# Performance work log

Measured on AMD Instinct MI355X. Metric: run time of the kernel, lower is better.

The kernel has to match this reference:

```python
import jax, jax.numpy as jnp
import numpy as np

B, S, E, H, D, W = 2, 4096, 768, 12, 64, 256  # batch, seq, hidden, heads, head_dim, one-sided window


def setup_inputs() -> dict:
    key = jax.random.key(0)
    ks = jax.random.split(key, 4)
    s = 0.02
    return {
        "hidden_states": jax.random.normal(ks[0], (B, S, E), jnp.float32),
        "Wq": jax.random.normal(ks[1], (E, E), jnp.float32) * s,
        "bq": jnp.zeros((E,), jnp.float32),
        "Wk": jax.random.normal(ks[2], (E, E), jnp.float32) * s,
        "bk": jnp.zeros((E,), jnp.float32),
        "Wv": jax.random.normal(ks[3], (E, E), jnp.float32) * s,
        "bv": jnp.zeros((E,), jnp.float32),
    }


def _band_attention(q, k, v):
    # q,k,v: [B,H,S,D]. Sliding-window attention: query i attends keys j with |j-i| <= W,
    # clipped to [0, S) -- same math as sliding_chunks_matmul_qk + mask_invalid_locations
    # + softmax + sliding_chunks_matmul_pv (dropout p=0, eval mode).
    C = S // W  # number of query chunks of size W

    def ext(x):
        # gather, for each chunk c, the keys of chunks c-1, c, c+1 (zero padded at edges)
        xp = jnp.pad(x, ((0, 0), (0, 0), (W, W), (0, 0)))
        xc = xp.reshape(B, H, C + 2, W, D)
        return jnp.concatenate([xc[:, :, 0:C], xc[:, :, 1:C + 1], xc[:, :, 2:C + 2]], axis=3)  # [B,H,C,3W,D]

    qc = q.reshape(B, H, C, W, D)
    ke = ext(k)
    ve = ext(v)
    scores = jnp.einsum('bhcpd,bhctd->bhcpt', qc, ke)  # [B,H,C,W,3W]

    p = jnp.arange(W)[:, None]            # query offset within chunk
    t = jnp.arange(3 * W)[None, :]        # key offset within extended window
    rel = t - W - p                       # j - i  (relative position)
    j = jnp.arange(C)[:, None, None] * W + (t - W)[None]  # global key index [C,W,3W]
    mask = (jnp.abs(rel)[None] <= W) & (j >= 0) & (j < S)  # band + sequence-boundary mask

    scores = jnp.where(mask[None, None], scores, -1e30)
    probs = jax.nn.softmax(scores, axis=-1)
    out = jnp.einsum('bhcpt,bhctd->bhcpd', probs, ve)
    return out.reshape(B, H, S, D)


def reference(hidden_states, Wq, bq, Wk, bk, Wv, bv):
    scale = 1.0 / float(np.sqrt(D))
    q = (hidden_states @ Wq + bq) * scale  # q scaled by 1/sqrt(head_dim) as in original
    k = hidden_states @ Wk + bk
    v = hidden_states @ Wv + bv
    split = lambda x: x.reshape(B, S, H, D).transpose(0, 2, 1, 3)  # [B,H,S,D]
    out = _band_attention(split(q), split(k), split(v))
    return out.transpose(0, 2, 1, 3).reshape(B, S, E)  # [B,S,E] context_layer
```

## Files before the change

kernel.cpp:

```cpp
#include <hip/hip_runtime.h>

#define BB 2
#define SS 4096
#define EE 768
#define HH 12
#define DD 64
#define WW 256

typedef __attribute__((ext_vector_type(8))) short short8;
typedef __attribute__((ext_vector_type(4))) short short4v;
typedef __attribute__((ext_vector_type(4))) float floatx4;

#define MFMA16(a, b, c) __builtin_amdgcn_mfma_f32_16x16x32_bf16(a, b, c, 0, 0, 0)

__device__ __forceinline__ float bf2f(short x) {
    union { unsigned u; float f; } v;
    v.u = ((unsigned)(unsigned short)x) << 16;
    return v.f;
}

__device__ __forceinline__ short f2bf(float x) {
    union { float f; unsigned u; } v;
    v.f = x;
    unsigned r = v.u + 0x7fffu + ((v.u >> 16) & 1u);
    return (short)(r >> 16);
}

__device__ __forceinline__ int imin(int a, int b) { return a < b ? a : b; }
__device__ __forceinline__ int imax(int a, int b) { return a > b ? a : b; }

__device__ __forceinline__ void gload_lds16(const short* g, short* l) {
    __builtin_amdgcn_global_load_lds(
        (const __attribute__((address_space(1))) unsigned*)g,
        (__attribute__((address_space(3))) unsigned*)l, 16, 0, 0);
}

__global__ __launch_bounds__(256) void convert_x(const float* __restrict__ in,
                                                 short* __restrict__ out) {
    int i = blockIdx.x * 256 + threadIdx.x;
    const floatx4* src = (const floatx4*)(in + (size_t)i * 8);
    floatx4 f0 = src[0], f1 = src[1];
    short8 s8;
#pragma unroll
    for (int j = 0; j < 4; j++) { s8[j] = f2bf(f0[j]); s8[j + 4] = f2bf(f1[j]); }
    *(short8*)(out + (size_t)i * 8) = s8;
}

__global__ void transpose_w(const float* __restrict__ W0, const float* __restrict__ W1,
                            const float* __restrict__ W2, short* __restrict__ out) {
    __shared__ short t[32][33];
    int z = blockIdx.z;
    const float* in = (z == 0) ? W0 : (z == 1) ? W1 : W2;
    short* op = out + (size_t)z * EE * EE;
    int tx = threadIdx.x, ty = threadIdx.y;
    int x = blockIdx.x * 32 + tx;
    int y0 = blockIdx.y * 32;
    for (int j = 0; j < 32; j += 8) t[ty + j][tx] = f2bf(in[(size_t)(y0 + ty + j) * EE + x]);
    __syncthreads();
    int x2 = y0 + tx;
    int y2 = blockIdx.x * 32;
    for (int j = 0; j < 32; j += 8) op[(size_t)(y2 + ty + j) * EE + x2] = t[tx][ty + j];
}

__global__ __launch_bounds__(256) void qkv_gemm(
    const short* __restrict__ Xb, const short* __restrict__ Wt,
    const float* __restrict__ Bq, const float* __restrict__ Bk, const float* __restrict__ Bv,
    short* __restrict__ Qo, short* __restrict__ Ko, short* __restrict__ Vto) {
    int z = blockIdx.z;
    const short* Wz = Wt + (size_t)z * EE * EE;
    const float* bias = (z == 0) ? Bq : (z == 1) ? Bk : Bv;

    __shared__ __align__(16) short As[128 * 32];
    __shared__ __align__(16) short Bs[128 * 32];
    int tid = threadIdx.x;
    int m0 = blockIdx.x * 128, n0 = blockIdx.y * 128;
    int wave = tid >> 6, lane = tid & 63, lquad = lane >> 4, lrow = lane & 15;
    int wm = (wave & 1) * 64, wn = (wave >> 1) * 64;

    floatx4 acc[4][4] = {};

    int c0 = tid, c1 = 256 + tid;
    int r0s = c0 >> 2, c0s = (c0 & 3) * 8;
    int r1s = c1 >> 2, c1s = (c1 & 3) * 8;

    for (int k0 = 0; k0 < EE; k0 += 32) {
        gload_lds16(&Xb[(size_t)(m0 + r0s) * EE + k0 + c0s], &As[c0 * 8]);
        gload_lds16(&Wz[(size_t)(n0 + r0s) * EE + k0 + c0s], &Bs[c0 * 8]);
        gload_lds16(&Xb[(size_t)(m0 + r1s) * EE + k0 + c1s], &As[c1 * 8]);
        gload_lds16(&Wz[(size_t)(n0 + r1s) * EE + k0 + c1s], &Bs[c1 * 8]);
        __syncthreads();
        short8 af[4], bfv[4];
#pragma unroll
        for (int mt = 0; mt < 4; mt++)
            af[mt] = *(short8*)&As[(wm + mt * 16 + lrow) * 32 + lquad * 8];
#pragma unroll
        for (int nt = 0; nt < 4; nt++)
            bfv[nt] = *(short8*)&Bs[(wn + nt * 16 + lrow) * 32 + lquad * 8];
#pragma unroll
        for (int mt = 0; mt < 4; mt++)
#pragma unroll
            for (int nt = 0; nt < 4; nt++)
                acc[mt][nt] = MFMA16(af[mt], bfv[nt], acc[mt][nt]);
        __syncthreads();
    }

    if (z == 2) {
        for (int nt = 0; nt < 4; nt++) {
            int gn = n0 + wn + nt * 16 + lrow;
            float bv = bias[gn];
            int h = gn >> 6, d = gn & 63;
            for (int mt = 0; mt < 4; mt++) {
                int gm0 = m0 + wm + mt * 16 + lquad * 4;
                int b = gm0 >> 12, s = gm0 & (SS - 1);
                short4v pk;
                for (int r = 0; r < 4; r++) pk[r] = f2bf(acc[mt][nt][r] + bv);
                *(short4v*)&Vto[(((size_t)(b * HH + h)) * DD + d) * SS + s] = pk;
            }
        }
    } else {
        short* out = (z == 0) ? Qo : Ko;
        float scale = (z == 0) ? 0.125f : 1.0f;
        for (int nt = 0; nt < 4; nt++) {
            int gn = n0 + wn + nt * 16 + lrow;
            float bv = bias[gn];
            int h = gn >> 6, d = gn & 63;
            for (int mt = 0; mt < 4; mt++) {
                int gmb = m0 + wm + mt * 16 + lquad * 4;
                for (int r = 0; r < 4; r++) {
                    int gm = gmb + r;
                    int b = gm >> 12, s = gm & (SS - 1);
                    float v = (acc[mt][nt][r] + bv) * scale;
                    out[(((size_t)(b * HH + h)) * SS + s) * DD + d] = f2bf(v);
                }
            }
        }
    }
}

__global__ __launch_bounds__(256) void band_attn(
    const short* __restrict__ Q, const short* __restrict__ K,
    const short* __restrict__ Vt, float* __restrict__ out) {
    int hb = blockIdx.x;
    int h = hb % HH, b = hb / HH;
    int chunk = blockIdx.y;
    int tid = threadIdx.x;
    int wave = tid >> 6, lane = tid & 63, lquad = lane >> 4, lrow = lane & 15;
    int qbase = chunk * 128 + wave * 32;

    const short* Qh = Q + ((size_t)(b * HH + h)) * SS * DD;
    const short* Kh = K + ((size_t)(b * HH + h)) * SS * DD;
    const short* Vh = Vt + ((size_t)(b * HH + h)) * DD * SS;

    __shared__ __align__(16) short Ks[64 * 72];
    __shared__ __align__(16) short Vs[64 * 72];
    __shared__ __align__(16) short Ps[4][16 * 72];
    short* Pw = &Ps[wave][0];

    short8 qf[2][2];
#pragma unroll
    for (int m = 0; m < 2; m++)
#pragma unroll
        for (int hh = 0; hh < 2; hh++)
            qf[m][hh] = *(const short8*)&Qh[(size_t)(qbase + m * 16 + lrow) * DD + hh * 32 + lquad * 8];

    floatx4 o[2][4] = {};
    float ls[2] = {0.0f, 0.0f};

    int kwin = chunk * 128 - WW;
    int srow = tid >> 3;
    int scol = (tid & 7) * 8;
    int tlo = wave >> 1;

    for (int t = 0; t < 10; t++) {
        int ks0 = kwin + t * 64;
#pragma unroll
        for (int i = 0; i < 2; i++) {
            int r = srow + i * 32;
            int gk = imin(imax(ks0 + r, 0), SS - 1);
            *(short8*)&Ks[r * 72 + scol] = *(const short8*)&Kh[(size_t)gk * DD + scol];
            int gv = imin(imax(ks0 + scol, 0), SS - 8);
            *(short8*)&Vs[r * 72 + scol] = *(const short8*)&Vh[(size_t)r * SS + gv];
        }
        __syncthreads();

        if ((unsigned)(t - tlo) < 9u) {
            short8 kf[4][2], vf[4][2];
#pragma unroll
            for (int kt = 0; kt < 4; kt++)
#pragma unroll
                for (int hh = 0; hh < 2; hh++)
                    kf[kt][hh] = *(short8*)&Ks[(kt * 16 + lrow) * 72 + hh * 32 + lquad * 8];
#pragma unroll
            for (int nt = 0; nt < 4; nt++)
#pragma unroll
                for (int hh = 0; hh < 2; hh++)
                    vf[nt][hh] = *(short8*)&Vs[(nt * 16 + lrow) * 72 + hh * 32 + lquad * 8];

#pragma unroll
            for (int m = 0; m < 2; m++) {
                int q = qbase + m * 16 + lrow;
                floatx4 s[4];
#pragma unroll
                for (int kt = 0; kt < 4; kt++) {
                    floatx4 zz = {};
                    s[kt] = MFMA16(kf[kt][0], qf[m][0], zz);
                    s[kt] = MFMA16(kf[kt][1], qf[m][1], s[kt]);
                }
                float lacc = 0.0f;
#pragma unroll
                for (int kt = 0; kt < 4; kt++) {
                    short4v pk;
#pragma unroll
                    for (int r = 0; r < 4; r++) {
                        int key = ks0 + kt * 16 + lquad * 4 + r;
                        bool valid = ((unsigned)(key - q + WW) <= 2u * WW) && ((unsigned)key < SS);
                        float p = valid ? __expf(s[kt][r]) : 0.0f;
                        pk[r] = f2bf(p);
                        lacc += bf2f(pk[r]);
                    }
                    *(short4v*)&Pw[lrow * 72 + kt * 16 + lquad * 4] = pk;
                }
                ls[m] += lacc;
                asm volatile("" ::: "memory");
                short8 ap0 = *(short8*)&Pw[lrow * 72 + lquad * 8];
                short8 ap1 = *(short8*)&Pw[lrow * 72 + 32 + lquad * 8];
#pragma unroll
                for (int nt = 0; nt < 4; nt++) {
                    o[m][nt] = MFMA16(ap0, vf[nt][0], o[m][nt]);
                    o[m][nt] = MFMA16(ap1, vf[nt][1], o[m][nt]);
                }
            }
        }
        __syncthreads();
    }

#pragma unroll
    for (int m = 0; m < 2; m++) {
        ls[m] += __shfl_xor(ls[m], 16, 64);
        ls[m] += __shfl_xor(ls[m], 32, 64);
        ls[m] = 1.0f / ls[m];
    }

#pragma unroll
    for (int m = 0; m < 2; m++) {
#pragma unroll
        for (int r = 0; r < 4; r++) {
            float linv = __shfl(ls[m], lquad * 4 + r, 64);
            int s = qbase + m * 16 + lquad * 4 + r;
#pragma unroll
            for (int nt = 0; nt < 4; nt++)
                out[((size_t)b * SS + s) * EE + h * DD + nt * 16 + lrow] = o[m][nt][r] * linv;
        }
    }
}

extern "C" void kernel_launch(void* const* d_in, const int* in_sizes, int n_in,
                              void* d_out, int out_size, void* d_ws, size_t ws_size,
                              hipStream_t stream) {
    const float* hidden = (const float*)d_in[0];
    const float* Wq = (const float*)d_in[1];
    const float* bq = (const float*)d_in[2];
    const float* Wk = (const float*)d_in[3];
    const float* bk = (const float*)d_in[4];
    const float* Wv = (const float*)d_in[5];
    const float* bv = (const float*)d_in[6];
    float* out = (float*)d_out;

    short* ws = (short*)d_ws;
    const size_t WSZ = (size_t)EE * EE;
    const size_t QSZ = (size_t)BB * HH * SS * DD;
    short* Wt = ws;
    short* Qb = Wt + 3 * WSZ;
    short* Kb = Qb + QSZ;
    short* Vtb = Kb + QSZ;
    short* Xb = (short*)d_out;

    convert_x<<<dim3((BB * SS * EE) / (256 * 8), 1, 1), 256, 0, stream>>>(hidden, Xb);
    transpose_w<<<dim3(24, 24, 3), dim3(32, 8, 1), 0, stream>>>(Wq, Wk, Wv, Wt);

    qkv_gemm<<<dim3(64, 6, 3), 256, 0, stream>>>(Xb, Wt, bq, bk, bv, Qb, Kb, Vtb);

    band_attn<<<dim3(HH * BB, SS / 128, 1), 256, 0, stream>>>(Qb, Kb, Vtb, out);
}
```

Measured before the change: 185.3 us.

## Merge prep kernels and restructure QKV GEMM into single-wave double-buffered tiles

Result: slower. 196.7 us (+6.2%).

```diff
diff --git a/kernel.cpp b/kernel.cpp
--- a/kernel.cpp
+++ b/kernel.cpp
@@ -35,34 +35,36 @@
         (__attribute__((address_space(3))) unsigned*)l, 16, 0, 0);
 }
 
-__global__ __launch_bounds__(256) void convert_x(const float* __restrict__ in,
-                                                 short* __restrict__ out) {
-    int i = blockIdx.x * 256 + threadIdx.x;
-    const floatx4* src = (const floatx4*)(in + (size_t)i * 8);
-    floatx4 f0 = src[0], f1 = src[1];
-    short8 s8;
-#pragma unroll
-    for (int j = 0; j < 4; j++) { s8[j] = f2bf(f0[j]); s8[j + 4] = f2bf(f1[j]); }
-    *(short8*)(out + (size_t)i * 8) = s8;
-}
-
-__global__ void transpose_w(const float* __restrict__ W0, const float* __restrict__ W1,
-                            const float* __restrict__ W2, short* __restrict__ out) {
+__global__ __launch_bounds__(256) void prep(
+    const float* __restrict__ hidden, const float* __restrict__ W0,
+    const float* __restrict__ W1, const float* __restrict__ W2,
+    short* __restrict__ Xb, short* __restrict__ Wt) {
     __shared__ short t[32][33];
-    int z = blockIdx.z;
-    const float* in = (z == 0) ? W0 : (z == 1) ? W1 : W2;
-    short* op = out + (size_t)z * EE * EE;
-    int tx = threadIdx.x, ty = threadIdx.y;
-    int x = blockIdx.x * 32 + tx;
-    int y0 = blockIdx.y * 32;
-    for (int j = 0; j < 32; j += 8) t[ty + j][tx] = f2bf(in[(size_t)(y0 + ty + j) * EE + x]);
-    __syncthreads();
-    int x2 = y0 + tx;
-    int y2 = blockIdx.x * 32;
-    for (int j = 0; j < 32; j += 8) op[(size_t)(y2 + ty + j) * EE + x2] = t[tx][ty + j];
-}
-
-__global__ __launch_bounds__(256) void qkv_gemm(
+    int bid = blockIdx.x;
+    if (bid < 3072) {
+        int i = bid * 256 + threadIdx.x;
+        const floatx4* src = (const floatx4*)(hidden + (size_t)i * 8);
+        floatx4 f0 = src[0], f1 = src[1];
+        short8 s8;
+#pragma unroll
+        for (int j = 0; j < 4; j++) { s8[j] = f2bf(f0[j]); s8[j + 4] = f2bf(f1[j]); }
+        *(short8*)(Xb + (size_t)i * 8) = s8;
+    } else {
+        int tmp = bid - 3072;
+        int z = tmp / 576, r = tmp % 576;
+        int bx = r % 24, by = r / 24;
+        const float* in = (z == 0) ? W0 : (z == 1) ? W1 : W2;
+        short* op = Wt + (size_t)z * EE * EE;
+        int tx = threadIdx.x & 31, ty = threadIdx.x >> 5;
+        int x = bx * 32 + tx, y0 = by * 32;
+        for (int j = 0; j < 32; j += 8) t[ty + j][tx] = f2bf(in[(size_t)(y0 + ty + j) * EE + x]);
+        __syncthreads();
+        int x2 = y0 + tx, y2 = bx * 32;
+        for (int j = 0; j < 32; j += 8) op[(size_t)(y2 + ty + j) * EE + x2] = t[tx][ty + j];
+    }
+}
+
+__global__ __launch_bounds__(64) void qkv_gemm(
     const short* __restrict__ Xb, const short* __restrict__ Wt,
     const float* __restrict__ Bq, const float* __restrict__ Bk, const float* __restrict__ Bv,
     short* __restrict__ Qo, short* __restrict__ Ko, short* __restrict__ Vto) {
@@ -70,47 +72,54 @@
     const short* Wz = Wt + (size_t)z * EE * EE;
     const float* bias = (z == 0) ? Bq : (z == 1) ? Bk : Bv;
 
-    __shared__ __align__(16) short As[128 * 32];
-    __shared__ __align__(16) short Bs[128 * 32];
-    int tid = threadIdx.x;
-    int m0 = blockIdx.x * 128, n0 = blockIdx.y * 128;
-    int wave = tid >> 6, lane = tid & 63, lquad = lane >> 4, lrow = lane & 15;
-    int wm = (wave & 1) * 64, wn = (wave >> 1) * 64;
+    __shared__ __align__(16) short As[2][64 * 32];
+    __shared__ __align__(16) short Bs[2][64 * 32];
+    int lane = threadIdx.x;
+    int m0 = blockIdx.x * 64, n0 = blockIdx.y * 64;
+    int lquad = lane >> 4, lrow = lane & 15;
 
     floatx4 acc[4][4] = {};
 
-    int c0 = tid, c1 = 256 + tid;
-    int r0s = c0 >> 2, c0s = (c0 & 3) * 8;
-    int r1s = c1 >> 2, c1s = (c1 & 3) * 8;
-
-    for (int k0 = 0; k0 < EE; k0 += 32) {
-        gload_lds16(&Xb[(size_t)(m0 + r0s) * EE + k0 + c0s], &As[c0 * 8]);
-        gload_lds16(&Wz[(size_t)(n0 + r0s) * EE + k0 + c0s], &Bs[c0 * 8]);
-        gload_lds16(&Xb[(size_t)(m0 + r1s) * EE + k0 + c1s], &As[c1 * 8]);
-        gload_lds16(&Wz[(size_t)(n0 + r1s) * EE + k0 + c1s], &Bs[c1 * 8]);
-        __syncthreads();
+    auto stage = [&](int k0, int buf) {
+#pragma unroll
+        for (int j = 0; j < 4; j++) {
+            int c = j * 64 + lane;
+            int row = c >> 2, col = (c & 3) * 8;
+            gload_lds16(&Xb[(size_t)(m0 + row) * EE + k0 + col], &As[buf][c * 8]);
+            gload_lds16(&Wz[(size_t)(n0 + row) * EE + k0 + col], &Bs[buf][c * 8]);
+        }
+    };
+
+    stage(0, 0);
+    for (int i = 0; i < 24; i++) {
+        int buf = i & 1;
+        if (i < 23) {
+            stage((i + 1) * 32, buf ^ 1);
+            asm volatile("s_waitcnt vmcnt(8)" ::: "memory");
+        } else {
+            asm volatile("s_waitcnt vmcnt(0)" ::: "memory");
+        }
         short8 af[4], bfv[4];
 #pragma unroll
         for (int mt = 0; mt < 4; mt++)
-            af[mt] = *(short8*)&As[(wm + mt * 16 + lrow) * 32 + lquad * 8];
+            af[mt] = *(short8*)&As[buf][(mt * 16 + lrow) * 32 + lquad * 8];
 #pragma unroll
         for (int nt = 0; nt < 4; nt++)
-            bfv[nt] = *(short8*)&Bs[(wn + nt * 16 + lrow) * 32 + lquad * 8];
+            bfv[nt] = *(short8*)&Bs[buf][(nt * 16 + lrow) * 32 + lquad * 8];
 #pragma unroll
         for (int mt = 0; mt < 4; mt++)
 #pragma unroll
             for (int nt = 0; nt < 4; nt++)
                 acc[mt][nt] = MFMA16(af[mt], bfv[nt], acc[mt][nt]);
-        __syncthreads();
     }
 
     if (z == 2) {
         for (int nt = 0; nt < 4; nt++) {
-            int gn = n0 + wn + nt * 16 + lrow;
+            int gn = n0 + nt * 16 + lrow;
             float bv = bias[gn];
             int h = gn >> 6, d = gn & 63;
             for (int mt = 0; mt < 4; mt++) {
-                int gm0 = m0 + wm + mt * 16 + lquad * 4;
+                int gm0 = m0 + mt * 16 + lquad * 4;
                 int b = gm0 >> 12, s = gm0 & (SS - 1);
                 short4v pk;
                 for (int r = 0; r < 4; r++) pk[r] = f2bf(acc[mt][nt][r] + bv);
@@ -121,11 +130,11 @@
         short* out = (z == 0) ? Qo : Ko;
         float scale = (z == 0) ? 0.125f : 1.0f;
         for (int nt = 0; nt < 4; nt++) {
-            int gn = n0 + wn + nt * 16 + lrow;
+            int gn = n0 + nt * 16 + lrow;
             float bv = bias[gn];
             int h = gn >> 6, d = gn & 63;
             for (int mt = 0; mt < 4; mt++) {
-                int gmb = m0 + wm + mt * 16 + lquad * 4;
+                int gmb = m0 + mt * 16 + lquad * 4;
                 for (int r = 0; r < 4; r++) {
                     int gm = gmb + r;
                     int b = gm >> 12, s = gm & (SS - 1);
@@ -275,10 +284,9 @@
     short* Vtb = Kb + QSZ;
     short* Xb = (short*)d_out;
 
-    convert_x<<<dim3((BB * SS * EE) / (256 * 8), 1, 1), 256, 0, stream>>>(hidden, Xb);
-    transpose_w<<<dim3(24, 24, 3), dim3(32, 8, 1), 0, stream>>>(Wq, Wk, Wv, Wt);
-
-    qkv_gemm<<<dim3(64, 6, 3), 256, 0, stream>>>(Xb, Wt, bq, bk, bv, Qb, Kb, Vtb);
+    prep<<<dim3(3072 + 3 * 576, 1, 1), 256, 0, stream>>>(hidden, Wq, Wk, Wv, Xb, Wt);
+
+    qkv_gemm<<<dim3(128, 12, 3), 64, 0, stream>>>(Xb, Wt, bq, bk, bv, Qb, Kb, Vtb);
 
     band_attn<<<dim3(HH * BB, SS / 128, 1), 256, 0, stream>>>(Qb, Kb, Vtb, out);
 }
```

## Double-buffer K/V tiles in band attention, skip masks on interior tiles, fuse prep kernels

Applied to the files above, without the earlier changes.

Result: faster. 181.3 us (-2.2%).

```diff
diff --git a/kernel.cpp b/kernel.cpp
--- a/kernel.cpp
+++ b/kernel.cpp
@@ -35,31 +35,33 @@
         (__attribute__((address_space(3))) unsigned*)l, 16, 0, 0);
 }
 
-__global__ __launch_bounds__(256) void convert_x(const float* __restrict__ in,
-                                                 short* __restrict__ out) {
-    int i = blockIdx.x * 256 + threadIdx.x;
-    const floatx4* src = (const floatx4*)(in + (size_t)i * 8);
-    floatx4 f0 = src[0], f1 = src[1];
-    short8 s8;
-#pragma unroll
-    for (int j = 0; j < 4; j++) { s8[j] = f2bf(f0[j]); s8[j + 4] = f2bf(f1[j]); }
-    *(short8*)(out + (size_t)i * 8) = s8;
-}
-
-__global__ void transpose_w(const float* __restrict__ W0, const float* __restrict__ W1,
-                            const float* __restrict__ W2, short* __restrict__ out) {
+__global__ __launch_bounds__(256) void prep(
+    const float* __restrict__ hidden, const float* __restrict__ W0,
+    const float* __restrict__ W1, const float* __restrict__ W2,
+    short* __restrict__ Xb, short* __restrict__ Wt) {
     __shared__ short t[32][33];
-    int z = blockIdx.z;
-    const float* in = (z == 0) ? W0 : (z == 1) ? W1 : W2;
-    short* op = out + (size_t)z * EE * EE;
-    int tx = threadIdx.x, ty = threadIdx.y;
-    int x = blockIdx.x * 32 + tx;
-    int y0 = blockIdx.y * 32;
-    for (int j = 0; j < 32; j += 8) t[ty + j][tx] = f2bf(in[(size_t)(y0 + ty + j) * EE + x]);
-    __syncthreads();
-    int x2 = y0 + tx;
-    int y2 = blockIdx.x * 32;
-    for (int j = 0; j < 32; j += 8) op[(size_t)(y2 + ty + j) * EE + x2] = t[tx][ty + j];
+    int bid = blockIdx.x;
+    if (bid < 3072) {
+        int i = bid * 256 + threadIdx.x;
+        const floatx4* src = (const floatx4*)(hidden + (size_t)i * 8);
+        floatx4 f0 = src[0], f1 = src[1];
+        short8 s8;
+#pragma unroll
+        for (int j = 0; j < 4; j++) { s8[j] = f2bf(f0[j]); s8[j + 4] = f2bf(f1[j]); }
+        *(short8*)(Xb + (size_t)i * 8) = s8;
+    } else {
+        int tmp = bid - 3072;
+        int z = tmp / 576, r = tmp % 576;
+        int bx = r % 24, by = r / 24;
+        const float* in = (z == 0) ? W0 : (z == 1) ? W1 : W2;
+        short* op = Wt + (size_t)z * EE * EE;
+        int tx = threadIdx.x & 31, ty = threadIdx.x >> 5;
+        int x = bx * 32 + tx, y0 = by * 32;
+        for (int j = 0; j < 32; j += 8) t[ty + j][tx] = f2bf(in[(size_t)(y0 + ty + j) * EE + x]);
+        __syncthreads();
+        int x2 = y0 + tx, y2 = bx * 32;
+        for (int j = 0; j < 32; j += 8) op[(size_t)(y2 + ty + j) * EE + x2] = t[tx][ty + j];
+    }
 }
 
 __global__ __launch_bounds__(256) void qkv_gemm(
@@ -151,8 +153,8 @@
     const short* Kh = K + ((size_t)(b * HH + h)) * SS * DD;
     const short* Vh = Vt + ((size_t)(b * HH + h)) * DD * SS;
 
-    __shared__ __align__(16) short Ks[64 * 72];
-    __shared__ __align__(16) short Vs[64 * 72];
+    __shared__ __align__(16) short Ks[2][64 * 72];
+    __shared__ __align__(16) short Vs[2][64 * 72];
     __shared__ __align__(16) short Ps[4][16 * 72];
     short* Pw = &Ps[wave][0];
 
@@ -171,30 +173,51 @@
     int scol = (tid & 7) * 8;
     int tlo = wave >> 1;
 
-    for (int t = 0; t < 10; t++) {
+    short8 kreg[2], vreg[2];
+    auto loadTile = [&](int t) {
         int ks0 = kwin + t * 64;
 #pragma unroll
         for (int i = 0; i < 2; i++) {
             int r = srow + i * 32;
             int gk = imin(imax(ks0 + r, 0), SS - 1);
-            *(short8*)&Ks[r * 72 + scol] = *(const short8*)&Kh[(size_t)gk * DD + scol];
+            kreg[i] = *(const short8*)&Kh[(size_t)gk * DD + scol];
             int gv = imin(imax(ks0 + scol, 0), SS - 8);
-            *(short8*)&Vs[r * 72 + scol] = *(const short8*)&Vh[(size_t)r * SS + gv];
-        }
-        __syncthreads();
+            vreg[i] = *(const short8*)&Vh[(size_t)r * SS + gv];
+        }
+    };
+    auto storeTile = [&](int buf) {
+#pragma unroll
+        for (int i = 0; i < 2; i++) {
+            int r = srow + i * 32;
+            *(short8*)&Ks[buf][r * 72 + scol] = kreg[i];
+            *(short8*)&Vs[buf][r * 72 + scol] = vreg[i];
+        }
+    };
+
+    loadTile(0);
+    storeTile(0);
+    __syncthreads();
+
+    for (int t = 0; t < 10; t++) {
+        int buf = t & 1;
+        if (t < 9) loadTile(t + 1);
 
         if ((unsigned)(t - tlo) < 9u) {
+            int ks0 = kwin + t * 64;
             short8 kf[4][2], vf[4][2];
 #pragma unroll
             for (int kt = 0; kt < 4; kt++)
 #pragma unroll
                 for (int hh = 0; hh < 2; hh++)
-                    kf[kt][hh] = *(short8*)&Ks[(kt * 16 + lrow) * 72 + hh * 32 + lquad * 8];
+                    kf[kt][hh] = *(short8*)&Ks[buf][(kt * 16 + lrow) * 72 + hh * 32 + lquad * 8];
 #pragma unroll
             for (int nt = 0; nt < 4; nt++)
 #pragma unroll
                 for (int hh = 0; hh < 2; hh++)
-                    vf[nt][hh] = *(short8*)&Vs[(nt * 16 + lrow) * 72 + hh * 32 + lquad * 8];
+                    vf[nt][hh] = *(short8*)&Vs[buf][(nt * 16 + lrow) * 72 + hh * 32 + lquad * 8];
+
+            int d0 = ks0 - qbase;
+            bool interior = (d0 >= -225) && (d0 <= 193) && (ks0 >= 0) && (ks0 <= SS - 64);
 
 #pragma unroll
             for (int m = 0; m < 2; m++) {
@@ -207,18 +230,32 @@
                     s[kt] = MFMA16(kf[kt][1], qf[m][1], s[kt]);
                 }
                 float lacc = 0.0f;
-#pragma unroll
-                for (int kt = 0; kt < 4; kt++) {
-                    short4v pk;
-#pragma unroll
-                    for (int r = 0; r < 4; r++) {
-                        int key = ks0 + kt * 16 + lquad * 4 + r;
-                        bool valid = ((unsigned)(key - q + WW) <= 2u * WW) && ((unsigned)key < SS);
-                        float p = valid ? __expf(s[kt][r]) : 0.0f;
-                        pk[r] = f2bf(p);
-                        lacc += bf2f(pk[r]);
+                if (interior) {
+#pragma unroll
+                    for (int kt = 0; kt < 4; kt++) {
+                        short4v pk;
+#pragma unroll
+                        for (int r = 0; r < 4; r++) {
+                            float p = __expf(s[kt][r]);
+                            pk[r] = f2bf(p);
+                            lacc += bf2f(pk[r]);
+                        }
+                        *(short4v*)&Pw[lrow * 72 + kt * 16 + lquad * 4] = pk;
                     }
-                    *(short4v*)&Pw[lrow * 72 + kt * 16 + lquad * 4] = pk;
+                } else {
+#pragma unroll
+                    for (int kt = 0; kt < 4; kt++) {
+                        short4v pk;
+#pragma unroll
+                        for (int r = 0; r < 4; r++) {
+                            int key = ks0 + kt * 16 + lquad * 4 + r;
+                            bool valid = ((unsigned)(key - q + WW) <= 2u * WW) && ((unsigned)key < SS);
+                            float p = valid ? __expf(s[kt][r]) : 0.0f;
+                            pk[r] = f2bf(p);
+                            lacc += bf2f(pk[r]);
+                        }
+                        *(short4v*)&Pw[lrow * 72 + kt * 16 + lquad * 4] = pk;
+                    }
                 }
                 ls[m] += lacc;
                 asm volatile("" ::: "memory");
@@ -231,6 +268,8 @@
                 }
             }
         }
+
+        if (t < 9) storeTile(buf ^ 1);
         __syncthreads();
     }
 
@@ -275,8 +314,7 @@
     short* Vtb = Kb + QSZ;
     short* Xb = (short*)d_out;
 
-    convert_x<<<dim3((BB * SS * EE) / (256 * 8), 1, 1), 256, 0, stream>>>(hidden, Xb);
-    transpose_w<<<dim3(24, 24, 3), dim3(32, 8, 1), 0, stream>>>(Wq, Wk, Wv, Wt);
+    prep<<<dim3(3072 + 3 * 576, 1, 1), 256, 0, stream>>>(hidden, Wq, Wk, Wv, Xb, Wt);
 
     qkv_gemm<<<dim3(64, 6, 3), 256, 0, stream>>>(Xb, Wt, bq, bk, bv, Qb, Kb, Vtb);
 
```
